# Kernel tuning notes

Measured on AMD Instinct MI355X. Metric: run time of the kernel, lower is better.

Reference implementation:

```python
import jax, jax.numpy as jnp
import numpy as np
from jax import lax

B, L = 4, 512
D_MODEL, D_STATE, D_CONV, EXPAND = 1024, 16, 4, 2
D_INNER = EXPAND * D_MODEL
DT_RANK = (D_MODEL + 15) // 16  # math.ceil(d_model / 16) = 64


def setup_inputs() -> dict:
    key = jax.random.key(0)
    ks = jax.random.split(key, 16)

    def rn(k, shape, scale=1.0):
        return jax.random.normal(k, shape, jnp.float32) * scale

    # A initialized as log(1..d_state) broadcast over d_inner, as in the module
    A_log = jnp.log(jnp.broadcast_to(jnp.arange(1, D_STATE + 1, dtype=jnp.float32), (D_INNER, D_STATE)))
    return {
        "hidden_states": rn(ks[0], (B, L, D_MODEL)),
        "in_proj_w": rn(ks[1], (2 * D_INNER, D_MODEL), D_MODEL ** -0.5),
        "conv1d_w": rn(ks[2], (D_INNER, 1, D_CONV), D_CONV ** -0.5),
        "conv1d_bias": rn(ks[3], (D_INNER,), 0.02),
        "x_proj_w": rn(ks[4], (DT_RANK + 2 * D_STATE, D_INNER), D_INNER ** -0.5),
        "dt_proj_w": rn(ks[5], (D_INNER, DT_RANK), DT_RANK ** -0.5),
        "dt_proj_bias": rn(ks[6], (D_INNER,), 0.02) - 4.0,
        "A_log": A_log,
        "D": jnp.ones((D_INNER,), jnp.float32),
        "conv1d_b_w": rn(ks[7], (D_INNER, 1, D_CONV), D_CONV ** -0.5),
        "conv1d_b_bias": rn(ks[8], (D_INNER,), 0.02),
        "x_proj_b_w": rn(ks[9], (DT_RANK + 2 * D_STATE, D_INNER), D_INNER ** -0.5),
        "dt_proj_b_w": rn(ks[10], (D_INNER, DT_RANK), DT_RANK ** -0.5),
        "dt_proj_b_bias": rn(ks[11], (D_INNER,), 0.02) - 4.0,
        "A_b_log": A_log,
        "D_b": jnp.ones((D_INNER,), jnp.float32),
        "out_proj_w": rn(ks[12], (D_MODEL, D_INNER), D_INNER ** -0.5),
    }


def _selective_scan(u, delta, A, Bm, Cm, Dv):
    # u, delta: [b,l,d]; Bm, Cm: [b,l,n]; A: [d,n]; Dv: [d]
    # h_t = exp(delta_t * A) * h_{t-1} + delta_t * B_t * u_t ; y_t = <h_t, C_t> + D * u_t
    def step(h, inp):
        u_t, dt_t, B_t, C_t = inp  # [b,d], [b,d], [b,n], [b,n]
        dA = jnp.exp(dt_t[:, :, None] * A)  # [b,d,n]
        h = dA * h + (dt_t * u_t)[:, :, None] * B_t[:, None, :]
        y = jnp.einsum('bdn,bn->bd', h, C_t)
        return h, y

    b, l, d = u.shape
    h0 = jnp.zeros((b, d, A.shape[1]), u.dtype)
    xs = (u.transpose(1, 0, 2), delta.transpose(1, 0, 2), Bm.transpose(1, 0, 2), Cm.transpose(1, 0, 2))
    _, ys = lax.scan(step, h0, xs)  # ys: [l,b,d]
    return ys.transpose(1, 0, 2) + u * Dv


def _direction(x_bdl, conv_w, conv_b, xproj_w, dtproj_w, dtproj_b, A_log, Dv):
    # x_bdl: [b, d_inner, l]. torch pads both sides with d_conv-1 then slices [:L] -> causal depthwise conv.
    xc = lax.conv_general_dilated(x_bdl, conv_w, (1,), [(D_CONV - 1, 0)],
                                  dimension_numbers=('NCH', 'OIH', 'NCH'),
                                  feature_group_count=D_INNER)
    xc = (xc + conv_b[None, :, None]).transpose(0, 2, 1)  # [b,l,d_inner]
    x_dbl = xc @ xproj_w.T  # [b,l,dt_rank+2n]
    dt = x_dbl[..., :DT_RANK] @ dtproj_w.T + dtproj_b
    Bm = x_dbl[..., DT_RANK:DT_RANK + D_STATE]
    Cm = x_dbl[..., DT_RANK + D_STATE:]
    xc = jnp.clip(xc, -10.0, 10.0)
    dt = jnp.clip(dt, 1e-5, 1.0)
    # source passes dt_proj.bias again as delta_bias with delta_softplus=True (bias added twice; faithful)
    delta = jax.nn.softplus(dt + dtproj_b)
    A = -jnp.exp(A_log)
    return _selective_scan(xc, delta, A, Bm, Cm, Dv)


def reference(hidden_states, in_proj_w, conv1d_w, conv1d_bias, x_proj_w, dt_proj_w, dt_proj_bias,
              A_log, D, conv1d_b_w, conv1d_b_bias, x_proj_b_w, dt_proj_b_w, dt_proj_b_bias,
              A_b_log, D_b, out_proj_w):
    xz = (hidden_states @ in_proj_w.T).transpose(0, 2, 1)  # [b, 2*d_inner, l]
    x, z = jnp.split(xz, 2, axis=1)  # each [b, d_inner, l]
    y_fwd = _direction(x, conv1d_w, conv1d_bias, x_proj_w, dt_proj_w, dt_proj_bias, A_log, D)
    y_bwd = _direction(x[:, :, ::-1], conv1d_b_w, conv1d_b_bias, x_proj_b_w, dt_proj_b_w,
                       dt_proj_b_bias, A_b_log, D_b)[:, ::-1, :]  # flip back along seq
    y = (y_fwd + y_bwd) * jax.nn.silu(z.transpose(0, 2, 1))  # [b,l,d_inner]
    out = y @ out_proj_w.T  # [b,l,d_model]
    return jnp.nan_to_num(out, nan=0.0, posinf=1.0, neginf=-1.0)
```

## Files before the change

kernel.cpp:

```cpp
#include <hip/hip_runtime.h>
#include <hip/hip_bf16.h>
#include <math.h>

#define BB 4
#define LL 512
#define DMODEL 1024
#define DSTATE 16
#define DCONV 4
#define DINNER 2048
#define DTRANK 64
#define MROWS (BB*LL)
#define G2KS 4
#define SCHUNK 32
#define SNC (LL / SCHUNK)

typedef __hip_bfloat16 bf16;
typedef __attribute__((ext_vector_type(8))) short short8;
typedef __attribute__((ext_vector_type(4))) short short4v;
typedef __attribute__((ext_vector_type(4))) float f32x4;

__device__ __forceinline__ float softplusf(float x) {
    return x > 20.f ? x : log1pf(__expf(x));
}

__device__ __forceinline__ void stage16(const void* g, void* l) {
    __builtin_amdgcn_global_load_lds(
        (const __attribute__((address_space(1))) void*)g,
        (__attribute__((address_space(3))) void*)l, 16, 0, 0);
}

__device__ __forceinline__ bool a_is_arange(const float* Aa) {
    bool ok = true;
#pragma unroll
    for (int n = 1; n < DSTATE; ++n) {
        float k = (float)(n + 1);
        ok = ok && (fabsf(Aa[n] - k * Aa[0]) <= 1e-4f * k * fabsf(Aa[0]));
    }
    return ok;
}

__global__ __launch_bounds__(256) void gemm_bf16(
    const bf16* __restrict__ A, const bf16* __restrict__ W,
    bf16* __restrict__ C, int N, int K, int lda, int ldw, int ldc)
{
    __shared__ bf16 lA[2][128 * 32];
    __shared__ bf16 lW[2][128 * 32];

    const int tid = threadIdx.x;
    const int lane = tid & 63;
    const int wid = tid >> 6;
    const int wr = wid >> 1;
    const int wc = wid & 1;
    const int rowBase = blockIdx.y * 128;
    const int colBase = blockIdx.x * 128;

    const int r16 = lane & 15;
    const int kg = lane >> 4;
    const int srow = (lane >> 2);
    const int scol = (lane & 3) * 8;

    f32x4 acc[4][4];
#pragma unroll
    for (int m = 0; m < 4; ++m)
#pragma unroll
        for (int n = 0; n < 4; ++n) acc[m][n] = (f32x4)0.f;

    for (int k0 = 0; k0 < K; k0 += 64) {
#pragma unroll
        for (int h = 0; h < 2; ++h) {
#pragma unroll
            for (int c = 0; c < 2; ++c) {
                int r = wid * 32 + c * 16 + srow;
                stage16(&A[(size_t)(rowBase + r) * lda + k0 + h * 32 + scol],
                        &lA[h][(wid * 32 + c * 16) * 32]);
                stage16(&W[(size_t)(colBase + r) * ldw + k0 + h * 32 + scol],
                        &lW[h][(wid * 32 + c * 16) * 32]);
            }
        }
        __syncthreads();

#pragma unroll
        for (int h = 0; h < 2; ++h) {
            short8 a[4], b[4];
#pragma unroll
            for (int m = 0; m < 4; ++m)
                a[m] = *(const short8*)&lA[h][(wr * 64 + m * 16 + r16) * 32 + kg * 8];
#pragma unroll
            for (int n = 0; n < 4; ++n)
                b[n] = *(const short8*)&lW[h][(wc * 64 + n * 16 + r16) * 32 + kg * 8];
#pragma unroll
            for (int m = 0; m < 4; ++m)
#pragma unroll
                for (int n = 0; n < 4; ++n)
                    acc[m][n] = __builtin_amdgcn_mfma_f32_16x16x32_bf16(
                        a[m], b[n], acc[m][n], 0, 0, 0);
        }
        __syncthreads();
    }

#pragma unroll
    for (int m = 0; m < 4; ++m) {
#pragma unroll
        for (int n = 0; n < 4; ++n) {
            int gc = colBase + wc * 64 + n * 16 + r16;
#pragma unroll
            for (int j = 0; j < 4; ++j) {
                int gr = rowBase + wr * 64 + m * 16 + kg * 4 + j;
                C[(size_t)gr * ldc + gc] = __float2bfloat16(acc[m][n][j]);
            }
        }
    }
}

__global__ __launch_bounds__(256) void g4_mfma(
    const bf16* __restrict__ A, const bf16* __restrict__ W,
    float* __restrict__ part)
{
    const int kz = blockIdx.z;
    const int kOff = kz * 1024;
    float* C = part + (size_t)kz * 2048 * 1024;

    __shared__ bf16 lA[2][128 * 32];
    __shared__ bf16 lW[2][128 * 32];

    const int tid = threadIdx.x;
    const int lane = tid & 63;
    const int wid = tid >> 6;
    const int wr = wid >> 1;
    const int wc = wid & 1;
    const int rowBase = blockIdx.y * 128;
    const int colBase = blockIdx.x * 128;

    const int r16 = lane & 15;
    const int kg = lane >> 4;
    const int srow = (lane >> 2);
    const int scol = (lane & 3) * 8;

    f32x4 acc[4][4];
#pragma unroll
    for (int m = 0; m < 4; ++m)
#pragma unroll
        for (int n = 0; n < 4; ++n) acc[m][n] = (f32x4)0.f;

    for (int k0 = 0; k0 < 1024; k0 += 64) {
#pragma unroll
        for (int h = 0; h < 2; ++h) {
#pragma unroll
            for (int c = 0; c < 2; ++c) {
                int r = wid * 32 + c * 16 + srow;
                stage16(&A[(size_t)(rowBase + r) * 2048 + kOff + k0 + h * 32 + scol],
                        &lA[h][(wid * 32 + c * 16) * 32]);
                stage16(&W[(size_t)(colBase + r) * 2048 + kOff + k0 + h * 32 + scol],
                        &lW[h][(wid * 32 + c * 16) * 32]);
            }
        }
        __syncthreads();

#pragma unroll
        for (int h = 0; h < 2; ++h) {
            short8 a[4], b[4];
#pragma unroll
            for (int m = 0; m < 4; ++m)
                a[m] = *(const short8*)&lA[h][(wr * 64 + m * 16 + r16) * 32 + kg * 8];
#pragma unroll
            for (int n = 0; n < 4; ++n)
                b[n] = *(const short8*)&lW[h][(wc * 64 + n * 16 + r16) * 32 + kg * 8];
#pragma unroll
            for (int m = 0; m < 4; ++m)
#pragma unroll
                for (int n = 0; n < 4; ++n)
                    acc[m][n] = __builtin_amdgcn_mfma_f32_16x16x32_bf16(
                        a[m], b[n], acc[m][n], 0, 0, 0);
        }
        __syncthreads();
    }

#pragma unroll
    for (int m = 0; m < 4; ++m) {
#pragma unroll
        for (int n = 0; n < 4; ++n) {
            int gc = colBase + wc * 64 + n * 16 + r16;
#pragma unroll
            for (int j = 0; j < 4; ++j) {
                int gr = rowBase + wr * 64 + m * 16 + kg * 4 + j;
                C[(size_t)gr * 1024 + gc] = acc[m][n][j];
            }
        }
    }
}

__global__ __launch_bounds__(256) void g4_reduce(
    const float* __restrict__ part, float* __restrict__ out)
{
    int i = (blockIdx.x * 256 + threadIdx.x) * 4;
    float4 p0 = *(const float4*)&part[i];
    float4 p1 = *(const float4*)&part[2048 * 1024 + i];
    float r[4] = { p0.x + p1.x, p0.y + p1.y, p0.z + p1.z, p0.w + p1.w };
#pragma unroll
    for (int j = 0; j < 4; ++j) {
        float v = r[j];
        if (isnan(v)) v = 0.f;
        else if (isinf(v)) v = (v > 0.f) ? 1.f : -1.f;
        r[j] = v;
    }
    *(float4*)&out[i] = *(float4*)r;
}

__global__ __launch_bounds__(256) void g3_mfma(
    const bf16* __restrict__ xdbl_bf,
    const bf16* __restrict__ dtw_bf,
    const float* __restrict__ biasf, const float* __restrict__ biasb,
    bf16* __restrict__ of, bf16* __restrict__ ob)
{
    const int dir = blockIdx.z;
    const bf16* A = xdbl_bf + (size_t)dir * 2048 * 96;
    const bf16* W = dtw_bf + (size_t)dir * 2048 * 64;
    const float* bias = dir ? biasb : biasf;
    bf16* C = dir ? ob : of;

    __shared__ bf16 lA[2][128 * 32];
    __shared__ bf16 lW[2][128 * 32];

    const int tid = threadIdx.x;
    const int lane = tid & 63;
    const int wid = tid >> 6;
    const int wr = wid >> 1;
    const int wc = wid & 1;
    const int rowBase = blockIdx.y * 128;
    const int colBase = blockIdx.x * 128;

    const int r16 = lane & 15;
    const int kg = lane >> 4;
    const int srow = (lane >> 2);
    const int scol = (lane & 3) * 8;

    f32x4 acc[4][4];
#pragma unroll
    for (int m = 0; m < 4; ++m)
#pragma unroll
        for (int n = 0; n < 4; ++n) acc[m][n] = (f32x4)0.f;

#pragma unroll
    for (int h = 0; h < 2; ++h) {
#pragma unroll
        for (int c = 0; c < 2; ++c) {
            int r = wid * 32 + c * 16 + srow;
            stage16(&A[(size_t)(rowBase + r) * 96 + h * 32 + scol],
                    &lA[h][(wid * 32 + c * 16) * 32]);
            stage16(&W[(size_t)(colBase + r) * 64 + h * 32 + scol],
                    &lW[h][(wid * 32 + c * 16) * 32]);
        }
    }
    __syncthreads();

#pragma unroll
    for (int h = 0; h < 2; ++h) {
        short8 a[4], b[4];
#pragma unroll
        for (int m = 0; m < 4; ++m)
            a[m] = *(const short8*)&lA[h][(wr * 64 + m * 16 + r16) * 32 + kg * 8];
#pragma unroll
        for (int n = 0; n < 4; ++n)
            b[n] = *(const short8*)&lW[h][(wc * 64 + n * 16 + r16) * 32 + kg * 8];
#pragma unroll
        for (int m = 0; m < 4; ++m)
#pragma unroll
            for (int n = 0; n < 4; ++n)
                acc[m][n] = __builtin_amdgcn_mfma_f32_16x16x32_bf16(
                    a[m], b[n], acc[m][n], 0, 0, 0);
    }

#pragma unroll
    for (int m = 0; m < 4; ++m) {
#pragma unroll
        for (int n = 0; n < 4; ++n) {
            int gc = colBase + wc * 64 + n * 16 + r16;
            float bv = bias[gc];
#pragma unroll
            for (int j = 0; j < 4; ++j) {
                int gr = rowBase + wr * 64 + m * 16 + kg * 4 + j;
                float t = acc[m][n][j] + bv;
                t = fminf(fmaxf(t, 1e-5f), 1.0f);
                C[(size_t)gr * 2048 + gc] = __float2bfloat16(softplusf(t + bv));
            }
        }
    }
}

__global__ __launch_bounds__(256) void g2_mfma(
    const bf16* __restrict__ xcbf_f, const bf16* __restrict__ xcbf_b,
    const bf16* __restrict__ wxf, const bf16* __restrict__ wxb,
    float* __restrict__ part)
{
    const int dir = blockIdx.z;
    const bf16* A = dir ? xcbf_b : xcbf_f;
    const bf16* W = dir ? wxb : wxf;
    const int rowBase = blockIdx.x * 128;
    const int kz = blockIdx.y;
    const int kBase = kz * (2048 / G2KS);

    __shared__ bf16 lA[128 * 40];
    __shared__ bf16 lW[96 * 40];

    const int tid = threadIdx.x;
    const int lane = tid & 63;
    const int wid = tid >> 6;
    const int r16 = lane & 15;
    const int kg = lane >> 4;

    f32x4 acc[2][6];
#pragma unroll
    for (int m = 0; m < 2; ++m)
#pragma unroll
        for (int n = 0; n < 6; ++n) acc[m][n] = (f32x4)0.f;

    const int srow = tid >> 2;
    const int scol = (tid & 3) * 8;

    for (int k0 = 0; k0 < 2048 / G2KS; k0 += 32) {
#pragma unroll
        for (int it = 0; it < 2; ++it) {
            int r = srow + it * 64;
            short8 va = *(const short8*)&A[(size_t)(rowBase + r) * 2048 + kBase + k0 + scol];
            *(short8*)&lA[r * 40 + scol] = va;
        }
        {
            short8 vw = *(const short8*)&W[(size_t)srow * 2048 + kBase + k0 + scol];
            *(short8*)&lW[srow * 40 + scol] = vw;
        }
        if (tid < 128) {
            int r = 64 + (tid >> 2);
            short8 vw2 = *(const short8*)&W[(size_t)r * 2048 + kBase + k0 + scol];
            *(short8*)&lW[r * 40 + scol] = vw2;
        }
        __syncthreads();

        short8 a[2], b[6];
#pragma unroll
        for (int m = 0; m < 2; ++m)
            a[m] = *(const short8*)&lA[(wid * 32 + m * 16 + r16) * 40 + kg * 8];
#pragma unroll
        for (int n = 0; n < 6; ++n)
            b[n] = *(const short8*)&lW[(n * 16 + r16) * 40 + kg * 8];
#pragma unroll
        for (int m = 0; m < 2; ++m)
#pragma unroll
            for (int n = 0; n < 6; ++n)
                acc[m][n] = __builtin_amdgcn_mfma_f32_16x16x32_bf16(
                    a[m], b[n], acc[m][n], 0, 0, 0);
        __syncthreads();
    }

    float* p = part + ((size_t)(dir * G2KS + kz) * 2048) * 96;
#pragma unroll
    for (int m = 0; m < 2; ++m) {
#pragma unroll
        for (int n = 0; n < 6; ++n) {
            int gc = n * 16 + r16;
#pragma unroll
            for (int j = 0; j < 4; ++j) {
                int gr = rowBase + wid * 32 + m * 16 + kg * 4 + j;
                p[(size_t)gr * 96 + gc] = acc[m][n][j];
            }
        }
    }
}

__global__ __launch_bounds__(256) void g2_reduce(
    const float* __restrict__ part, float* __restrict__ xf, float* __restrict__ xb,
    bf16* __restrict__ xdbl_bf)
{
    int idx = blockIdx.x * 256 + threadIdx.x;
    int c = idx % 96;
    int r = (idx / 96) & 2047;
    int dir = idx / (96 * 2048);
    float s = 0.f;
#pragma unroll
    for (int ks = 0; ks < G2KS; ++ks)
        s += part[((size_t)(dir * G2KS + ks) * 2048 + r) * 96 + c];
    (dir ? xb : xf)[(size_t)r * 96 + c] = s;
    xdbl_bf[((size_t)dir * 2048 + r) * 96 + c] = __float2bfloat16(s);
}

__global__ __launch_bounds__(256) void cast_all(
    const float* __restrict__ hidden, const float* __restrict__ in_proj_w,
    const float* __restrict__ xproj_w, const float* __restrict__ xproj_bw,
    const float* __restrict__ dtproj_w, const float* __restrict__ dtproj_bw,
    bf16* __restrict__ hbf, bf16* __restrict__ wbf,
    bf16* __restrict__ wxf, bf16* __restrict__ wxb,
    bf16* __restrict__ dtwf, bf16* __restrict__ dtwb)
{
    int bid = blockIdx.x;
    const float* src; bf16* dst; int base;
    if (bid < 1024)      { src = hidden;    dst = hbf;  base = bid; }
    else if (bid < 3072) { src = in_proj_w; dst = wbf;  base = bid - 1024; }
    else if (bid < 3168) { src = xproj_w;   dst = wxf;  base = bid - 3072; }
    else if (bid < 3264) { src = xproj_bw;  dst = wxb;  base = bid - 3168; }
    else if (bid < 3328) { src = dtproj_w;  dst = dtwf; base = bid - 3264; }
    else                 { src = dtproj_bw; dst = dtwb; base = bid - 3328; }
    int i = (base * 256 + threadIdx.x) * 8;
    float4 x = *(const float4*)&src[i];
    float4 y = *(const float4*)&src[i + 4];
    bf16 t[8] = { __float2bfloat16(x.x), __float2bfloat16(x.y),
                  __float2bfloat16(x.z), __float2bfloat16(x.w),
                  __float2bfloat16(y.x), __float2bfloat16(y.y),
                  __float2bfloat16(y.z), __float2bfloat16(y.w) };
    *(short8*)&dst[i] = *(short8*)t;
}

__global__ __launch_bounds__(256) void conv_kernel(
    const bf16* __restrict__ xz,
    const float* __restrict__ wf, const float* __restrict__ bf,
    const float* __restrict__ wb, const float* __restrict__ bb,
    bf16* __restrict__ xcbf, bf16* __restrict__ xcbb)
{
    int idx = blockIdx.x * 256 + threadIdx.x;
    int dg = idx & 511;
    int rest = idx >> 9;
    int l = rest & (LL - 1);
    int b = (rest >> 9) & (BB - 1);
    int dir = rest >> 11;
    int d0 = dg * 4;

    const float* w = dir ? wb : wf;
    const float* bias = dir ? bb : bf;

    float4 wv[4];
#pragma unroll
    for (int c = 0; c < 4; ++c)
        wv[c] = *(const float4*)&w[(d0 + c) * DCONV];

    float4 acc = *(const float4*)&bias[d0];
#pragma unroll
    for (int k = 0; k < DCONV; ++k) {
        int j = l - (DCONV - 1) + k;
        if (j >= 0) {
            int jj = dir ? (LL - 1 - j) : j;
            short4v xv = *(const short4v*)&xz[((size_t)(b * LL + jj)) * (2 * DINNER) + d0];
            const bf16* xp = (const bf16*)&xv;
            acc.x += ((const float*)&wv[0])[k] * __bfloat162float(xp[0]);
            acc.y += ((const float*)&wv[1])[k] * __bfloat162float(xp[1]);
            acc.z += ((const float*)&wv[2])[k] * __bfloat162float(xp[2]);
            acc.w += ((const float*)&wv[3])[k] * __bfloat162float(xp[3]);
        }
    }

    size_t off = ((size_t)(b * LL + l)) * DINNER + d0;
    bf16 t[4] = { __float2bfloat16(acc.x), __float2bfloat16(acc.y),
                  __float2bfloat16(acc.z), __float2bfloat16(acc.w) };
    *(short4v*)&((dir ? xcbb : xcbf)[off]) = *(short4v*)t;
}

__global__ __launch_bounds__(256) void scan1_kernel(
    const float* __restrict__ Alog_f, const float* __restrict__ Alog_b,
    const float* __restrict__ xdbl_f, const float* __restrict__ xdbl_b,
    const bf16* __restrict__ xc_f, const bf16* __restrict__ xc_b,
    const bf16* __restrict__ dl_f, const bf16* __restrict__ dl_b,
    float* __restrict__ sdel, float* __restrict__ hend)
{
    const int tid = threadIdx.x;
    const int d = blockIdx.x * 256 + tid;
    const int c = blockIdx.y;
    const int z = blockIdx.z;
    const int dir = z >> 2, b = z & 3;

    const float* Alog = dir ? Alog_b : Alog_f;
    const float* xdbl = dir ? xdbl_b : xdbl_f;
    const bf16* xc    = dir ? xc_b   : xc_f;
    const bf16* dl    = dir ? dl_b   : dl_f;
    const int rowBase = b * LL + c * SCHUNK;

    __shared__ float bs[SCHUNK][16];
#pragma unroll
    for (int i = 0; i < SCHUNK * 16 / 256; ++i) {
        int e = tid + 256 * i;
        int r = e >> 4, n = e & 15;
        bs[r][n] = xdbl[(size_t)(rowBase + r) * 96 + DTRANK + n];
    }
    __syncthreads();

    float Aa[DSTATE], h[DSTATE];
#pragma unroll
    for (int n = 0; n < DSTATE; ++n) {
        Aa[n] = -__expf(Alog[d * DSTATE + n]);
        h[n] = 0.f;
    }
    float sd = 0.f;
    const bool fast = a_is_arange(Aa);
    const float a0l2 = Aa[0] * 1.44269504f;

    float nxd = __bfloat162float(dl[(size_t)rowBase * DINNER + d]);
    float nxu = __bfloat162float(xc[(size_t)rowBase * DINNER + d]);

    if (fast) {
#pragma unroll 4
        for (int t = 0; t < SCHUNK; ++t) {
            float delta = nxd, u = nxu;
            if (t + 1 < SCHUNK) {
                size_t nrow = (size_t)(rowBase + t + 1);
                nxd = __bfloat162float(dl[nrow * DINNER + d]);
                nxu = __bfloat162float(xc[nrow * DINNER + d]);
            }
            u = fminf(fmaxf(u, -10.f), 10.f);
            float du = delta * u;
            sd += delta;
            float p[DSTATE];
            p[0] = exp2f(delta * a0l2);
#pragma unroll
            for (int n = 1; n < DSTATE; ++n)
                p[n] = p[n >> 1] * p[(n - 1) >> 1];
#pragma unroll
            for (int n = 0; n < DSTATE; ++n)
                h[n] = p[n] * h[n] + du * bs[t][n];
        }
    } else {
#pragma unroll 4
        for (int t = 0; t < SCHUNK; ++t) {
            float delta = nxd, u = nxu;
            if (t + 1 < SCHUNK) {
                size_t nrow = (size_t)(rowBase + t + 1);
                nxd = __bfloat162float(dl[nrow * DINNER + d]);
                nxu = __bfloat162float(xc[nrow * DINNER + d]);
            }
            u = fminf(fmaxf(u, -10.f), 10.f);
            float du = delta * u;
            sd += delta;
#pragma unroll
            for (int n = 0; n < DSTATE; ++n)
                h[n] = __expf(delta * Aa[n]) * h[n] + du * bs[t][n];
        }
    }

    size_t base = (size_t)z * SNC + c;
    sdel[base * DINNER + d] = sd;
#pragma unroll
    for (int n = 0; n < DSTATE; ++n)
        hend[(base * DSTATE + n) * DINNER + d] = h[n];
}

__global__ __launch_bounds__(256) void scan_combine(
    const float* __restrict__ Alog_f, const float* __restrict__ Alog_b,
    const float* __restrict__ sdel, float* __restrict__ hend)
{
    int g = blockIdx.x * 256 + threadIdx.x;
    int d = g & (DINNER - 1);
    int n = (g >> 11) & (DSTATE - 1);
    int z = g >> 15;
    const float* Alog = (z >> 2) ? Alog_b : Alog_f;

    float Aa = -__expf(Alog[d * DSTATE + n]);
    float hr = 0.f;
    for (int c = 0; c < SNC; ++c) {
        size_t base = (size_t)z * SNC + c;
        size_t idx = (base * DSTATE + n) * DINNER + d;
        float he = hend[idx];
        hend[idx] = hr;
        float sd = sdel[base * DINNER + d];
        hr = __expf(sd * Aa) * hr + he;
    }
}

__global__ __launch_bounds__(256) void scan2_kernel(
    const float* __restrict__ Alog_f, const float* __restrict__ Alog_b,
    const float* __restrict__ Df, const float* __restrict__ Db,
    const float* __restrict__ xdbl_f, const float* __restrict__ xdbl_b,
    const bf16* __restrict__ xc_f, const bf16* __restrict__ xc_b,
    const float* __restrict__ hin,
    bf16* __restrict__ dl_f, bf16* __restrict__ dl_b)
{
    const int tid = threadIdx.x;
    const int d = blockIdx.x * 256 + tid;
    const int c = blockIdx.y;
    const int z = blockIdx.z;
    const int dir = z >> 2, b = z & 3;

    const float* Alog = dir ? Alog_b : Alog_f;
    const float* xdbl = dir ? xdbl_b : xdbl_f;
    const bf16* xc    = dir ? xc_b   : xc_f;
    bf16* dl          = dir ? dl_b   : dl_f;
    const int rowBase = b * LL + c * SCHUNK;

    __shared__ float bs[SCHUNK][32];
#pragma unroll
    for (int i = 0; i < SCHUNK * 32 / 256; ++i) {
        int e = tid + 256 * i;
        int r = e >> 5, n = e & 31;
        bs[r][n] = xdbl[(size_t)(rowBase + r) * 96 + DTRANK + n];
    }
    __syncthreads();

    float Dv = (dir ? Db : Df)[d];
    size_t base = (size_t)z * SNC + c;
    float Aa[DSTATE], h[DSTATE];
#pragma unroll
    for (int n = 0; n < DSTATE; ++n) {
        Aa[n] = -__expf(Alog[d * DSTATE + n]);
        h[n] = hin[(base * DSTATE + n) * DINNER + d];
    }
    const bool fast = a_is_arange(Aa);
    const float a0l2 = Aa[0] * 1.44269504f;

    float nxd = __bfloat162float(dl[(size_t)rowBase * DINNER + d]);
    float nxu = __bfloat162float(xc[(size_t)rowBase * DINNER + d]);

    if (fast) {
#pragma unroll 4
        for (int t = 0; t < SCHUNK; ++t) {
            float delta = nxd, u = nxu;
            if (t + 1 < SCHUNK) {
                size_t nrow = (size_t)(rowBase + t + 1);
                nxd = __bfloat162float(dl[nrow * DINNER + d]);
                nxu = __bfloat162float(xc[nrow * DINNER + d]);
            }
            u = fminf(fmaxf(u, -10.f), 10.f);
            float du = delta * u;
            float p[DSTATE];
            p[0] = exp2f(delta * a0l2);
#pragma unroll
            for (int n = 1; n < DSTATE; ++n)
                p[n] = p[n >> 1] * p[(n - 1) >> 1];
            float y = 0.f;
#pragma unroll
            for (int n = 0; n < DSTATE; ++n) {
                h[n] = p[n] * h[n] + du * bs[t][n];
                y += h[n] * bs[t][DSTATE + n];
            }
            dl[(size_t)(rowBase + t) * DINNER + d] = __float2bfloat16(y + u * Dv);
        }
    } else {
#pragma unroll 4
        for (int t = 0; t < SCHUNK; ++t) {
            float delta = nxd, u = nxu;
            if (t + 1 < SCHUNK) {
                size_t nrow = (size_t)(rowBase + t + 1);
                nxd = __bfloat162float(dl[nrow * DINNER + d]);
                nxu = __bfloat162float(xc[nrow * DINNER + d]);
            }
            u = fminf(fmaxf(u, -10.f), 10.f);
            float du = delta * u;
            float y = 0.f;
#pragma unroll
            for (int n = 0; n < DSTATE; ++n) {
                h[n] = __expf(delta * Aa[n]) * h[n] + du * bs[t][n];
                y += h[n] * bs[t][DSTATE + n];
            }
            dl[(size_t)(rowBase + t) * DINNER + d] = __float2bfloat16(y + u * Dv);
        }
    }
}

__global__ __launch_bounds__(256) void gate_cast(
    const bf16* __restrict__ yf, const bf16* __restrict__ yb,
    const bf16* __restrict__ xz, bf16* __restrict__ ytot,
    const float* __restrict__ out_pw, bf16* __restrict__ obf)
{
    int bid = blockIdx.x;
    if (bid < 16384) {
        int idx = bid * 256 + threadIdx.x;
        int d = idx & (DINNER - 1);
        int l = (idx >> 11) & (LL - 1);
        int b = idx >> 20;
        size_t rowf = (size_t)(b * LL + l);
        size_t rowb = (size_t)(b * LL + (LL - 1 - l));
        float y = __bfloat162float(yf[rowf * DINNER + d]) +
                  __bfloat162float(yb[rowb * DINNER + d]);
        float z = __bfloat162float(xz[rowf * (2 * DINNER) + DINNER + d]);
        float s = z / (1.f + __expf(-z));
        ytot[rowf * DINNER + d] = __float2bfloat16(y * s);
    } else {
        int i = ((bid - 16384) * 256 + threadIdx.x) * 8;
        float4 x = *(const float4*)&out_pw[i];
        float4 y = *(const float4*)&out_pw[i + 4];
        bf16 t[8] = { __float2bfloat16(x.x), __float2bfloat16(x.y),
                      __float2bfloat16(x.z), __float2bfloat16(x.w),
                      __float2bfloat16(y.x), __float2bfloat16(y.y),
                      __float2bfloat16(y.z), __float2bfloat16(y.w) };
        *(short8*)&obf[i] = *(short8*)t;
    }
}

extern "C" void kernel_launch(void* const* d_in, const int* in_sizes, int n_in,
                              void* d_out, int out_size, void* d_ws, size_t ws_size,
                              hipStream_t stream)
{
    const float* hidden    = (const float*)d_in[0];
    const float* in_proj_w = (const float*)d_in[1];
    const float* conv_w    = (const float*)d_in[2];
    const float* conv_b    = (const float*)d_in[3];
    const float* xproj_w   = (const float*)d_in[4];
    const float* dtproj_w  = (const float*)d_in[5];
    const float* dtproj_b  = (const float*)d_in[6];
    const float* A_log     = (const float*)d_in[7];
    const float* Dvec      = (const float*)d_in[8];
    const float* conv_bw   = (const float*)d_in[9];
    const float* conv_bb   = (const float*)d_in[10];
    const float* xproj_bw  = (const float*)d_in[11];
    const float* dtproj_bw = (const float*)d_in[12];
    const float* dtproj_bb = (const float*)d_in[13];
    const float* A_b_log   = (const float*)d_in[14];
    const float* D_b       = (const float*)d_in[15];
    const float* out_pw    = (const float*)d_in[16];
    float* out = (float*)d_out;

    float* ws = (float*)d_ws;
    float* xzR     = ws;
    float* xcR_f   = xzR + 8388608;
    float* xcR_b   = xcR_f + 4194304;
    float* xdbl_f  = xcR_b + 4194304;
    float* xdbl_b  = xdbl_f + 196608;
    float* dlR_f   = xdbl_b + 196608;
    float* dlR_b   = dlR_f + 4194304;
    float* g2part  = dlR_b + 4194304;
    float* sdel    = g2part + 1572864;
    float* hend    = sdel + 262144;
    float* smallb  = hend + 4194304;

    bf16* xzbf = (bf16*)xzR;
    bf16* xcbf = (bf16*)xcR_f;
    bf16* xcbb = (bf16*)xcR_b;
    bf16* dlbf_f = (bf16*)dlR_f;
    bf16* dlbf_b = (bf16*)dlR_b;
    bf16* hbf = (bf16*)dlR_f;
    bf16* wbf = (bf16*)(dlR_f + 1048576);
    bf16* wxf = (bf16*)dlR_b;
    bf16* wxb = (bf16*)(dlR_b + 98304);
    bf16* xdbl_bf = (bf16*)smallb;
    bf16* dtw_bf  = (bf16*)(smallb + 196608);
    bf16* ytot_bf = (bf16*)xcR_f;
    bf16* obf = (bf16*)xcR_b;
    float* g4part = dlR_f;

    dim3 blk(256);

    cast_all<<<dim3(3392), blk, 0, stream>>>(
        hidden, in_proj_w, xproj_w, xproj_bw, dtproj_w, dtproj_bw,
        hbf, wbf, wxf, wxb, dtw_bf, dtw_bf + 131072);

    gemm_bf16<<<dim3(4096 / 128, MROWS / 128), blk, 0, stream>>>(
        hbf, wbf, xzbf, 4096, 1024, 1024, 1024, 4096);

    conv_kernel<<<dim3(2 * BB * LL * DINNER / 4 / 256), blk, 0, stream>>>(
        xzbf, conv_w, conv_b, conv_bw, conv_bb, xcbf, xcbb);

    g2_mfma<<<dim3(16, G2KS, 2), blk, 0, stream>>>(
        xcbf, xcbb, wxf, wxb, g2part);
    g2_reduce<<<dim3(2 * 2048 * 96 / 256), blk, 0, stream>>>(
        g2part, xdbl_f, xdbl_b, xdbl_bf);

    g3_mfma<<<dim3(16, 16, 2), blk, 0, stream>>>(
        xdbl_bf, dtw_bf, dtproj_b, dtproj_bb, dlbf_f, dlbf_b);

    scan1_kernel<<<dim3(DINNER / 256, SNC, 8), blk, 0, stream>>>(
        A_log, A_b_log, xdbl_f, xdbl_b, xcbf, xcbb, dlbf_f, dlbf_b, sdel, hend);
    scan_combine<<<dim3(2 * BB * DSTATE * DINNER / 256), blk, 0, stream>>>(
        A_log, A_b_log, sdel, hend);
    scan2_kernel<<<dim3(DINNER / 256, SNC, 8), blk, 0, stream>>>(
        A_log, A_b_log, Dvec, D_b, xdbl_f, xdbl_b, xcbf, xcbb, hend, dlbf_f, dlbf_b);

    gate_cast<<<dim3(16384 + 1024), blk, 0, stream>>>(
        dlbf_f, dlbf_b, xzbf, ytot_bf, out_pw, obf);

    g4_mfma<<<dim3(1024 / 128, MROWS / 128, 2), blk, 0, stream>>>(
        ytot_bf, obf, g4part);
    g4_reduce<<<dim3(2048 * 1024 / 4 / 256), blk, 0, stream>>>(g4part, out);
}
```

Before: 212.0 us.

## Halve scan chunk, store chunk states in bf16, drop split-K in out_proj GEMM

The selective-scan chunk length drops from 32 to 16, so the two scan passes run twice as many parallel blocks with shorter serial loops. The inter-chunk state buffer becomes bf16 to offset the larger state traffic this creates. The output projection GEMM no longer splits K into partial sums that a separate reduce kernel adds; it uses a 128x64 tile over the full K and applies nan_to_num inline. This removes one launch and the fp32 partial round trip, at the cost of longer serial per-block K loops, a longer scan_combine chain, and lower precision in the carried states.

```diff
diff --git a/kernel.cpp b/kernel.cpp
--- a/kernel.cpp
+++ b/kernel.cpp
@@ -11,7 +11,7 @@
 #define DTRANK 64
 #define MROWS (BB*LL)
 #define G2KS 4
-#define SCHUNK 32
+#define SCHUNK 16
 #define SNC (LL / SCHUNK)
 
 typedef __hip_bfloat16 bf16;
@@ -112,16 +112,12 @@
     }
 }
 
-__global__ __launch_bounds__(256) void g4_mfma(
+__global__ __launch_bounds__(256) void g4_direct(
     const bf16* __restrict__ A, const bf16* __restrict__ W,
-    float* __restrict__ part)
-{
-    const int kz = blockIdx.z;
-    const int kOff = kz * 1024;
-    float* C = part + (size_t)kz * 2048 * 1024;
-
+    float* __restrict__ out)
+{
     __shared__ bf16 lA[2][128 * 32];
-    __shared__ bf16 lW[2][128 * 32];
+    __shared__ bf16 lW[2][64 * 32];
 
     const int tid = threadIdx.x;
     const int lane = tid & 63;
@@ -129,46 +125,47 @@
     const int wr = wid >> 1;
     const int wc = wid & 1;
     const int rowBase = blockIdx.y * 128;
-    const int colBase = blockIdx.x * 128;
+    const int colBase = blockIdx.x * 64;
 
     const int r16 = lane & 15;
     const int kg = lane >> 4;
     const int srow = (lane >> 2);
     const int scol = (lane & 3) * 8;
 
-    f32x4 acc[4][4];
+    f32x4 acc[4][2];
 #pragma unroll
     for (int m = 0; m < 4; ++m)
 #pragma unroll
-        for (int n = 0; n < 4; ++n) acc[m][n] = (f32x4)0.f;
-
-    for (int k0 = 0; k0 < 1024; k0 += 64) {
+        for (int n = 0; n < 2; ++n) acc[m][n] = (f32x4)0.f;
+
+    for (int k0 = 0; k0 < 2048; k0 += 64) {
 #pragma unroll
         for (int h = 0; h < 2; ++h) {
 #pragma unroll
             for (int c = 0; c < 2; ++c) {
                 int r = wid * 32 + c * 16 + srow;
-                stage16(&A[(size_t)(rowBase + r) * 2048 + kOff + k0 + h * 32 + scol],
+                stage16(&A[(size_t)(rowBase + r) * 2048 + k0 + h * 32 + scol],
                         &lA[h][(wid * 32 + c * 16) * 32]);
-                stage16(&W[(size_t)(colBase + r) * 2048 + kOff + k0 + h * 32 + scol],
-                        &lW[h][(wid * 32 + c * 16) * 32]);
-            }
+            }
+            int rw = wid * 16 + srow;
+            stage16(&W[(size_t)(colBase + rw) * 2048 + k0 + h * 32 + scol],
+                    &lW[h][(wid * 16) * 32]);
         }
         __syncthreads();
 
 #pragma unroll
         for (int h = 0; h < 2; ++h) {
-            short8 a[4], b[4];
+            short8 a[4], b[2];
 #pragma unroll
             for (int m = 0; m < 4; ++m)
                 a[m] = *(const short8*)&lA[h][(wr * 64 + m * 16 + r16) * 32 + kg * 8];
 #pragma unroll
-            for (int n = 0; n < 4; ++n)
-                b[n] = *(const short8*)&lW[h][(wc * 64 + n * 16 + r16) * 32 + kg * 8];
+            for (int n = 0; n < 2; ++n)
+                b[n] = *(const short8*)&lW[h][(wc * 32 + n * 16 + r16) * 32 + kg * 8];
 #pragma unroll
             for (int m = 0; m < 4; ++m)
 #pragma unroll
-                for (int n = 0; n < 4; ++n)
+                for (int n = 0; n < 2; ++n)
                     acc[m][n] = __builtin_amdgcn_mfma_f32_16x16x32_bf16(
                         a[m], b[n], acc[m][n], 0, 0, 0);
         }
@@ -178,32 +175,18 @@
 #pragma unroll
     for (int m = 0; m < 4; ++m) {
 #pragma unroll
-        for (int n = 0; n < 4; ++n) {
-            int gc = colBase + wc * 64 + n * 16 + r16;
+        for (int n = 0; n < 2; ++n) {
+            int gc = colBase + wc * 32 + n * 16 + r16;
 #pragma unroll
             for (int j = 0; j < 4; ++j) {
                 int gr = rowBase + wr * 64 + m * 16 + kg * 4 + j;
-                C[(size_t)gr * 1024 + gc] = acc[m][n][j];
-            }
-        }
-    }
-}
-
-__global__ __launch_bounds__(256) void g4_reduce(
-    const float* __restrict__ part, float* __restrict__ out)
-{
-    int i = (blockIdx.x * 256 + threadIdx.x) * 4;
-    float4 p0 = *(const float4*)&part[i];
-    float4 p1 = *(const float4*)&part[2048 * 1024 + i];
-    float r[4] = { p0.x + p1.x, p0.y + p1.y, p0.z + p1.z, p0.w + p1.w };
-#pragma unroll
-    for (int j = 0; j < 4; ++j) {
-        float v = r[j];
-        if (isnan(v)) v = 0.f;
-        else if (isinf(v)) v = (v > 0.f) ? 1.f : -1.f;
-        r[j] = v;
-    }
-    *(float4*)&out[i] = *(float4*)r;
+                float v = acc[m][n][j];
+                if (isnan(v)) v = 0.f;
+                else if (isinf(v)) v = (v > 0.f) ? 1.f : -1.f;
+                out[(size_t)gr * 1024 + gc] = v;
+            }
+        }
+    }
 }
 
 __global__ __launch_bounds__(256) void g3_mfma(
@@ -456,7 +439,7 @@
     const float* __restrict__ xdbl_f, const float* __restrict__ xdbl_b,
     const bf16* __restrict__ xc_f, const bf16* __restrict__ xc_b,
     const bf16* __restrict__ dl_f, const bf16* __restrict__ dl_b,
-    float* __restrict__ sdel, float* __restrict__ hend)
+    float* __restrict__ sdel, bf16* __restrict__ hend)
 {
     const int tid = threadIdx.x;
     const int d = blockIdx.x * 256 + tid;
@@ -471,9 +454,8 @@
     const int rowBase = b * LL + c * SCHUNK;
 
     __shared__ float bs[SCHUNK][16];
-#pragma unroll
-    for (int i = 0; i < SCHUNK * 16 / 256; ++i) {
-        int e = tid + 256 * i;
+    {
+        int e = tid;
         int r = e >> 4, n = e & 15;
         bs[r][n] = xdbl[(size_t)(rowBase + r) * 96 + DTRANK + n];
     }
@@ -535,12 +517,12 @@
     sdel[base * DINNER + d] = sd;
 #pragma unroll
     for (int n = 0; n < DSTATE; ++n)
-        hend[(base * DSTATE + n) * DINNER + d] = h[n];
+        hend[(base * DSTATE + n) * DINNER + d] = __float2bfloat16(h[n]);
 }
 
 __global__ __launch_bounds__(256) void scan_combine(
     const float* __restrict__ Alog_f, const float* __restrict__ Alog_b,
-    const float* __restrict__ sdel, float* __restrict__ hend)
+    const float* __restrict__ sdel, bf16* __restrict__ hend)
 {
     int g = blockIdx.x * 256 + threadIdx.x;
     int d = g & (DINNER - 1);
@@ -553,8 +535,8 @@
     for (int c = 0; c < SNC; ++c) {
         size_t base = (size_t)z * SNC + c;
         size_t idx = (base * DSTATE + n) * DINNER + d;
-        float he = hend[idx];
-        hend[idx] = hr;
+        float he = __bfloat162float(hend[idx]);
+        hend[idx] = __float2bfloat16(hr);
         float sd = sdel[base * DINNER + d];
         hr = __expf(sd * Aa) * hr + he;
     }
@@ -565,7 +547,7 @@
     const float* __restrict__ Df, const float* __restrict__ Db,
     const float* __restrict__ xdbl_f, const float* __restrict__ xdbl_b,
     const bf16* __restrict__ xc_f, const bf16* __restrict__ xc_b,
-    const float* __restrict__ hin,
+    const bf16* __restrict__ hin,
     bf16* __restrict__ dl_f, bf16* __restrict__ dl_b)
 {
     const int tid = threadIdx.x;
@@ -595,7 +577,7 @@
 #pragma unroll
     for (int n = 0; n < DSTATE; ++n) {
         Aa[n] = -__expf(Alog[d * DSTATE + n]);
-        h[n] = hin[(base * DSTATE + n) * DINNER + d];
+        h[n] = __bfloat162float(hin[(base * DSTATE + n) * DINNER + d]);
     }
     const bool fast = a_is_arange(Aa);
     const float a0l2 = Aa[0] * 1.44269504f;
@@ -711,9 +693,9 @@
     float* dlR_f   = xdbl_b + 196608;
     float* dlR_b   = dlR_f + 4194304;
     float* g2part  = dlR_b + 4194304;
-    float* sdel    = g2part + 1572864;
-    float* hend    = sdel + 262144;
-    float* smallb  = hend + 4194304;
+    float* sdelOld = g2part + 1572864;
+    float* hendR   = sdelOld + 262144;
+    float* smallb  = hendR + 4194304;
 
     bf16* xzbf = (bf16*)xzR;
     bf16* xcbf = (bf16*)xcR_f;
@@ -722,13 +704,14 @@
     bf16* dlbf_b = (bf16*)dlR_b;
     bf16* hbf = (bf16*)dlR_f;
     bf16* wbf = (bf16*)(dlR_f + 1048576);
+    float* sdel = dlR_f + 3145728;
     bf16* wxf = (bf16*)dlR_b;
     bf16* wxb = (bf16*)(dlR_b + 98304);
+    bf16* hendbf = (bf16*)hendR;
     bf16* xdbl_bf = (bf16*)smallb;
     bf16* dtw_bf  = (bf16*)(smallb + 196608);
     bf16* ytot_bf = (bf16*)xcR_f;
     bf16* obf = (bf16*)xcR_b;
-    float* g4part = dlR_f;
 
     dim3 blk(256);
 
@@ -751,16 +734,15 @@
         xdbl_bf, dtw_bf, dtproj_b, dtproj_bb, dlbf_f, dlbf_b);
 
     scan1_kernel<<<dim3(DINNER / 256, SNC, 8), blk, 0, stream>>>(
-        A_log, A_b_log, xdbl_f, xdbl_b, xcbf, xcbb, dlbf_f, dlbf_b, sdel, hend);
+        A_log, A_b_log, xdbl_f, xdbl_b, xcbf, xcbb, dlbf_f, dlbf_b, sdel, hendbf);
     scan_combine<<<dim3(2 * BB * DSTATE * DINNER / 256), blk, 0, stream>>>(
-        A_log, A_b_log, sdel, hend);
+        A_log, A_b_log, sdel, hendbf);
     scan2_kernel<<<dim3(DINNER / 256, SNC, 8), blk, 0, stream>>>(
-        A_log, A_b_log, Dvec, D_b, xdbl_f, xdbl_b, xcbf, xcbb, hend, dlbf_f, dlbf_b);
+        A_log, A_b_log, Dvec, D_b, xdbl_f, xdbl_b, xcbf, xcbb, hendbf, dlbf_f, dlbf_b);
 
     gate_cast<<<dim3(16384 + 1024), blk, 0, stream>>>(
         dlbf_f, dlbf_b, xzbf, ytot_bf, out_pw, obf);
 
-    g4_mfma<<<dim3(1024 / 128, MROWS / 128, 2), blk, 0, stream>>>(
-        ytot_bf, obf, g4part);
-    g4_reduce<<<dim3(2048 * 1024 / 4 / 256), blk, 0, stream>>>(g4part, out);
-}
+    g4_direct<<<dim3(1024 / 64, MROWS / 128), blk, 0, stream>>>(
+        ytot_bf, obf, out);
+}
```

Result: no change. 214.1 us (+1.0%).
